# Optimization experiments

Hardware: AMD Instinct MI355X
Metric: run time of the kernel (lower is better)

Reference implementation:

```python
import jax, jax.numpy as jnp
import numpy as np

B, S, E, H = 2, 2048, 768, 8
D = E // H  # 96
SCALING = D ** (-0.5)


def setup_inputs() -> dict:
    key = jax.random.key(0)
    ks = jax.random.split(key, 7)
    sd = E ** -0.5
    return {
        "x": jax.random.normal(ks[0], (B, S, E), jnp.float32),
        "Wq": jax.random.normal(ks[1], (E, E), jnp.float32) * sd,
        "bq": jax.random.normal(ks[2], (E,), jnp.float32) * 0.02,
        "Wk": jax.random.normal(ks[3], (E, E), jnp.float32) * sd,
        "bk": jax.random.normal(ks[4], (E,), jnp.float32) * 0.02,
        "Wo": jax.random.normal(ks[5], (E, E), jnp.float32) * sd,
        "bo": jax.random.normal(ks[6], (E,), jnp.float32) * 0.02,
    }


def _split_heads(t):
    # [B, S, E] -> [B, H, S, D]
    return t.reshape(B, S, H, D).transpose(0, 2, 1, 3)


def reference(x, Wq, bq, Wk, bk, Wo, bo):
    q = _split_heads(x @ Wq + bq)
    k = _split_heads(x @ Wk + bk)
    # NOTE: faithful to source bug — values use the KEY projection
    v = _split_heads(x @ Wk + bk)
    energies = jnp.einsum("bhqd,bhkd->bhqk", q, k)  # [B,H,S,S]
    # NOTE: faithful to source — scaling applied AFTER softmax
    attn = jax.nn.softmax(energies, axis=-1) * SCALING
    out = jnp.einsum("bhqk,bhkd->bhqd", attn, v)
    out = out.transpose(0, 2, 1, 3).reshape(B, S, E)
    return out @ Wo + bo
```

## Files before the change

kernel.cpp:

```cpp
#include <hip/hip_runtime.h>
#include <hip/hip_bf16.h>
#include <math.h>
#include <stdint.h>

#define B_DIM 2
#define S_DIM 2048
#define E_DIM 768
#define H_DIM 8
#define D_DIM 96
#define M_DIM (B_DIM*S_DIM)
#define SCALE_F 0.10206207261596575f
#define LOG2E_F 1.44269504088896341f

typedef _Float16 f16x8 __attribute__((ext_vector_type(8)));
typedef float    f32x4  __attribute__((ext_vector_type(4)));
typedef float    f32x16 __attribute__((ext_vector_type(16)));
typedef unsigned int u32x4 __attribute__((ext_vector_type(4)));

#define MFMA16H(a,b,c) __builtin_amdgcn_mfma_f32_16x16x32_f16(a,b,c,0,0,0)
#define MFMA32H(a,b,c) __builtin_amdgcn_mfma_f32_32x32x16_f16(a,b,c,0,0,0)

__device__ inline unsigned short f2h(float f) {
    return __builtin_bit_cast(unsigned short, (_Float16)f);
}

__device__ inline unsigned pk2(float a, float b) {
    return __builtin_bit_cast(unsigned, __builtin_amdgcn_cvt_pkrtz(a, b));
}

__device__ inline void gload16(const void* g, void* l) {
    auto gp = reinterpret_cast<const __attribute__((address_space(1))) uint32_t*>(
        reinterpret_cast<uintptr_t>(g));
    auto lp = reinterpret_cast<__attribute__((address_space(3))) uint32_t*>(
        reinterpret_cast<uintptr_t>(l));
    __builtin_amdgcn_global_load_lds(gp, lp, 16, 0, 0);
}

__global__ __launch_bounds__(256) void prep_kernel(
    const float* __restrict__ X,
    const float* __restrict__ W0, const float* __restrict__ W1,
    const float* __restrict__ W2,
    unsigned short* __restrict__ Xf,
    unsigned short* __restrict__ T0, unsigned short* __restrict__ T1,
    unsigned short* __restrict__ T2)
{
    const int tid = threadIdx.x;
    if (blockIdx.x < 3072) {
        int i = (blockIdx.x * 256 + tid) * 4;
        float4 v = *(const float4*)(X + i);
        ushort4 h;
        h.x = f2h(v.x); h.y = f2h(v.y); h.z = f2h(v.z); h.w = f2h(v.w);
        *(ushort4*)(Xf + i) = h;
        return;
    }
    int idx = blockIdx.x - 3072;
    int z = idx / 144, rem = idx % 144;
    const float* W; unsigned short* T;
    if (z == 0)      { W = W0; T = T0; }
    else if (z == 1) { W = W1; T = T1; }
    else             { W = W2; T = T2; }
    const float sc = (z == 0) ? LOG2E_F : 1.0f;
    int k0 = (rem / 12) << 6, n0 = (rem % 12) << 6;

    __shared__ float tile[64][65];
    const int r = tid >> 4, c4 = (tid & 15) << 2;
    #pragma unroll
    for (int i = 0; i < 4; ++i) {
        float4 v = *(const float4*)(W + (size_t)(k0 + r + i*16)*E_DIM + n0 + c4);
        tile[r + i*16][c4+0] = v.x; tile[r + i*16][c4+1] = v.y;
        tile[r + i*16][c4+2] = v.z; tile[r + i*16][c4+3] = v.w;
    }
    __syncthreads();
    #pragma unroll
    for (int i = 0; i < 4; ++i) {
        int n = r + i*16;
        ushort4 h;
        h.x = f2h(tile[c4+0][n] * sc); h.y = f2h(tile[c4+1][n] * sc);
        h.z = f2h(tile[c4+2][n] * sc); h.w = f2h(tile[c4+3][n] * sc);
        *(ushort4*)(T + (size_t)(n0 + n)*E_DIM + k0 + c4) = h;
    }
}

__global__ __launch_bounds__(256) void gemm_qk_kernel(
    const unsigned short* __restrict__ A, const unsigned short* __restrict__ Bt,
    const float* __restrict__ bq, const float* __restrict__ bk,
    unsigned short* __restrict__ Qf, unsigned short* __restrict__ Kf)
{
    __shared__ unsigned short sA[2*8192];
    __shared__ unsigned short sB[2*4096];

    const int tid  = threadIdx.x;
    const int lane = tid & 63;
    const int w    = tid >> 6;
    const int qn   = lane & 15, quad = lane >> 4;
    const int wm   = w & 1, wn = w >> 1;

    const int flat = blockIdx.x;
    const int g = flat & 7, s = flat >> 3;
    const int row0 = ((g << 2) + (s & 3)) << 7;
    const int col0 = (s >> 2) << 6;

    const int ar = tid >> 2;
    const int ak = (tid & 3) << 3;

    const unsigned short* gA = A  + (size_t)(row0 + ar)*E_DIM + ak;
    const unsigned short* gB = Bt + (size_t)(col0 + ar)*E_DIM + ak;

    f32x4 acc[4][2];
    #pragma unroll
    for (int mt = 0; mt < 4; ++mt)
        #pragma unroll
        for (int nt = 0; nt < 2; ++nt)
            { acc[mt][nt][0]=0.f; acc[mt][nt][1]=0.f; acc[mt][nt][2]=0.f; acc[mt][nt][3]=0.f; }

    gload16(gA,                 sA + tid*8);
    gload16(gA + 64*E_DIM,      sA + 2048 + tid*8);
    gload16(gA + 32,            sA + 4096 + tid*8);
    gload16(gA + 64*E_DIM + 32, sA + 6144 + tid*8);
    gload16(gB,                 sB + tid*8);
    gload16(gB + 32,            sB + 2048 + tid*8);
    __syncthreads();

    for (int it = 0; it < 12; ++it) {
        const int cur = it & 1, nb = cur ^ 1;
        if (it < 11) {
            const int kn = (it + 1) << 6;
            gload16(gA + kn,                 sA + nb*8192 + tid*8);
            gload16(gA + 64*E_DIM + kn,      sA + nb*8192 + 2048 + tid*8);
            gload16(gA + kn + 32,            sA + nb*8192 + 4096 + tid*8);
            gload16(gA + 64*E_DIM + kn + 32, sA + nb*8192 + 6144 + tid*8);
            gload16(gB + kn,                 sB + nb*4096 + tid*8);
            gload16(gB + kn + 32,            sB + nb*4096 + 2048 + tid*8);
        }

        #pragma unroll
        for (int kk = 0; kk < 2; ++kk) {
            f16x8 af[4], bf[2];
            #pragma unroll
            for (int mt = 0; mt < 4; ++mt)
                af[mt] = *(const f16x8*)
                    &sA[cur*8192 + kk*4096 + (wm*64 + mt*16 + qn)*32 + quad*8];
            #pragma unroll
            for (int nt = 0; nt < 2; ++nt)
                bf[nt] = *(const f16x8*)
                    &sB[cur*4096 + kk*2048 + (wn*32 + nt*16 + qn)*32 + quad*8];
            #pragma unroll
            for (int mt = 0; mt < 4; ++mt)
                #pragma unroll
                for (int nt = 0; nt < 2; ++nt)
                    acc[mt][nt] = MFMA16H(af[mt], bf[nt], acc[mt][nt]);
        }
        __syncthreads();
    }

    #pragma unroll
    for (int nt = 0; nt < 2; ++nt) {
        int n = col0 + wn*32 + nt*16 + qn;
        bool isQ = n < E_DIM;
        float bias = isQ ? bq[n] * LOG2E_F : bk[n - E_DIM];
        unsigned short* op = isQ ? Qf : Kf;
        int nc = isQ ? n : n - E_DIM;
        #pragma unroll
        for (int mt = 0; mt < 4; ++mt)
            #pragma unroll
            for (int r = 0; r < 4; ++r) {
                int m = row0 + wm*64 + mt*16 + quad*4 + r;
                op[(size_t)m*E_DIM + nc] = f2h(acc[mt][nt][r] + bias);
            }
    }
}

__global__ __launch_bounds__(256) void attn_mfma_kernel(
    const unsigned short* __restrict__ Qf, const unsigned short* __restrict__ Kf,
    unsigned short* __restrict__ O0, unsigned short* __restrict__ O1,
    float2* __restrict__ ml)
{
    __shared__ unsigned short sKh[2][64][104];
    __shared__ unsigned short sKt[2][96][72];

    const int tid  = threadIdx.x;
    const int w    = tid >> 6;
    const int lane = tid & 63;
    const int col  = lane & 31;
    const int half = lane >> 5;
    const int b    = blockIdx.z >> 1;
    const int kh   = blockIdx.z & 1;
    const int h    = blockIdx.y;
    const int q0   = blockIdx.x << 7;
    const int key0 = kh << 10;

    f16x8 qf[6];
    {
        const size_t ro = ((size_t)(b*S_DIM + q0 + w*32 + col))*E_DIM
                          + h*D_DIM + half*8;
        #pragma unroll
        for (int kc = 0; kc < 6; ++kc)
            qf[kc] = *(const f16x8*)(Qf + ro + kc*16);
    }

    f32x16 o[3];
    #pragma unroll
    for (int nt = 0; nt < 3; ++nt)
        #pragma unroll
        for (int r = 0; r < 16; ++r) o[nt][r] = 0.f;
    float m_i = -INFINITY, l_i = 0.f;

    const bool stager = tid < 128;
    const int st = tid & 127;
    const int sp = st >> 2;
    const int dq = st & 3;
    const int kp2 = ((sp + ((dq & 1) << 4)) & 31) << 1;

    uint4 r0[3], r1[3];
    if (stager) {
        const size_t g0 = ((size_t)(b*S_DIM + key0 + 2*sp))*E_DIM + h*D_DIM + dq*8;
        #pragma unroll
        for (int i = 0; i < 3; ++i) {
            r0[i] = *(const uint4*)(Kf + g0 + 32*i);
            r1[i] = *(const uint4*)(Kf + g0 + E_DIM + 32*i);
        }
    }

    const int kswz = ((col >> 3) & 1) << 2;

    for (int kt = 0; kt < 16; ++kt) {
        const int p = kt & 1;
        if (stager) {
            #pragma unroll
            for (int i = 0; i < 3; ++i) {
                *(uint4*)&sKh[p][2*sp  ][dq*8 + 32*i] = r0[i];
                *(uint4*)&sKh[p][2*sp+1][dq*8 + 32*i] = r1[i];
            }
            const unsigned short* p0 = (const unsigned short*)r0;
            const unsigned short* p1 = (const unsigned short*)r1;
            #pragma unroll
            for (int c = 0; c < 24; ++c) {
                int d = dq*8 + ((c >> 3) << 5) + (c & 7);
                unsigned pk = (unsigned)p0[c] | ((unsigned)p1[c] << 16);
                *(unsigned*)&sKt[p][d][kp2] = pk;
            }
        }
        __syncthreads();

        if (stager && kt + 1 < 16) {
            const size_t g0 = ((size_t)(b*S_DIM + key0 + (kt+1)*64 + 2*sp))*E_DIM
                              + h*D_DIM + dq*8;
            #pragma unroll
            for (int i = 0; i < 3; ++i) {
                r0[i] = *(const uint4*)(Kf + g0 + 32*i);
                r1[i] = *(const uint4*)(Kf + g0 + E_DIM + 32*i);
            }
        }

        f32x16 s[2];
        __builtin_amdgcn_s_setprio(1);
        #pragma unroll
        for (int mt = 0; mt < 2; ++mt) {
            f32x16 acc;
            #pragma unroll
            for (int r = 0; r < 16; ++r) acc[r] = 0.f;
            #pragma unroll
            for (int kc = 0; kc < 6; ++kc) {
                f16x8 ah = *(const f16x8*)&sKh[p][mt*32 + col][kc*16 + half*8];
                acc = MFMA32H(ah, qf[kc], acc);
            }
            s[mt] = acc;
        }
        __builtin_amdgcn_s_setprio(0);

        float t[8];
        #pragma unroll
        for (int r = 0; r < 8; ++r)
            t[r] = fmaxf(fmaxf(s[0][r], s[0][r+8]), fmaxf(s[1][r], s[1][r+8]));
        float mx = fmaxf(fmaxf(fmaxf(t[0], t[1]), fmaxf(t[2], t[3])),
                         fmaxf(fmaxf(t[4], t[5]), fmaxf(t[6], t[7])));
        mx = fmaxf(mx, __shfl_xor(mx, 32));

        if (__any(mx > m_i + 10.0f)) {
            float m_new = fmaxf(m_i, mx);
            float alpha = __builtin_amdgcn_exp2f(m_i - m_new);
            l_i *= alpha;
            #pragma unroll
            for (int nt = 0; nt < 3; ++nt)
                #pragma unroll
                for (int r = 0; r < 16; ++r) o[nt][r] *= alpha;
            m_i = m_new;
        }

        #pragma unroll
        for (int mt = 0; mt < 2; ++mt)
            #pragma unroll
            for (int r = 0; r < 16; ++r)
                s[mt][r] = __builtin_amdgcn_exp2f(s[mt][r] - m_i);

        float a[8];
        #pragma unroll
        for (int r = 0; r < 8; ++r)
            a[r] = (s[0][r] + s[0][r+8]) + (s[1][r] + s[1][r+8]);
        float ps = ((a[0]+a[1]) + (a[2]+a[3])) + ((a[4]+a[5]) + (a[6]+a[7]));
        ps += __shfl_xor(ps, 32);
        l_i = l_i + ps;

        __builtin_amdgcn_s_setprio(1);
        #pragma unroll
        for (int kc = 0; kc < 4; ++kc) {
            const int mt = kc >> 1;
            const int g0 = (kc & 1) << 3;
            unsigned A0 = pk2(s[mt][g0+0], s[mt][g0+1]);
            unsigned A1 = pk2(s[mt][g0+2], s[mt][g0+3]);
            unsigned B0 = pk2(s[mt][g0+4], s[mt][g0+5]);
            unsigned B1 = pk2(s[mt][g0+6], s[mt][g0+7]);
            auto w0 = __builtin_amdgcn_permlane32_swap(A0, B0, false, false);
            auto w1 = __builtin_amdgcn_permlane32_swap(A1, B1, false, false);
            u32x4 pw;
            pw[0] = w0[0]; pw[1] = w1[0]; pw[2] = w0[1]; pw[3] = w1[1];
            f16x8 pb = __builtin_bit_cast(f16x8, pw);
            #pragma unroll
            for (int nt = 0; nt < 3; ++nt) {
                f16x8 va = *(const f16x8*)
                    &sKt[p][nt*32 + col][(((kc << 1) | half) ^ kswz) << 3];
                o[nt] = MFMA32H(va, pb, o[nt]);
            }
        }
        __builtin_amdgcn_s_setprio(0);
    }

    float inv = 1.0f / l_i;
    unsigned short* Ob = (kh ? O1 : O0)
        + ((size_t)(b*S_DIM + q0 + w*32 + col))*E_DIM + h*D_DIM;
    #pragma unroll
    for (int nt = 0; nt < 3; ++nt)
        #pragma unroll
        for (int rg = 0; rg < 4; ++rg) {
            ushort4 pk;
            pk.x = f2h(o[nt][4*rg+0]*inv); pk.y = f2h(o[nt][4*rg+1]*inv);
            pk.z = f2h(o[nt][4*rg+2]*inv); pk.w = f2h(o[nt][4*rg+3]*inv);
            *(ushort4*)(Ob + nt*32 + 8*rg + 4*half) = pk;
        }
    if (lane < 32) {
        int q = q0 + w*32 + lane;
        ml[((size_t)(kh*B_DIM + b)*H_DIM + h)*S_DIM + q] = make_float2(m_i, l_i);
    }
}

__device__ inline float2 mkscale(const float2* __restrict__ ml, int m, int h) {
    int b = m >> 11, q = m & (S_DIM - 1);
    float2 e0 = ml[((size_t)b*H_DIM + h)*S_DIM + q];
    float2 e1 = ml[((size_t)(B_DIM + b)*H_DIM + h)*S_DIM + q];
    float mm = fmaxf(e0.x, e1.x);
    float w0 = e0.y * __builtin_amdgcn_exp2f(e0.x - mm);
    float w1 = e1.y * __builtin_amdgcn_exp2f(e1.x - mm);
    float inv = SCALE_F / (w0 + w1);
    return make_float2(w0*inv, w1*inv);
}

__global__ __launch_bounds__(256) void gemm_out_kernel(
    const unsigned short* __restrict__ O0, const unsigned short* __restrict__ O1,
    const float2* __restrict__ ml, const unsigned short* __restrict__ Bt,
    const float* __restrict__ bo, float* __restrict__ out)
{
    __shared__ unsigned short sA[2*4096];
    __shared__ unsigned short sB[2*4096];

    const int tid  = threadIdx.x;
    const int lane = tid & 63;
    const int w    = tid >> 6;
    const int qn   = lane & 15, quad = lane >> 4;
    const int wm   = w & 1, wn = w >> 1;

    const int flat = blockIdx.x;
    const int g = flat & 7, s = flat >> 3;
    const int row0 = ((g << 3) + (s & 7)) << 6;
    const int col0 = (s >> 3) << 6;

    const int ar = tid >> 2;
    const int ak = (tid & 3) << 3;

    const size_t r0o = (size_t)(row0 + ar)*E_DIM;
    const unsigned short* gB = Bt + (size_t)(col0 + ar)*E_DIM + ak;

    f32x4 acc[2][2];
    #pragma unroll
    for (int mt = 0; mt < 2; ++mt)
        #pragma unroll
        for (int nt = 0; nt < 2; ++nt)
            { acc[mt][nt][0]=0.f; acc[mt][nt][1]=0.f; acc[mt][nt][2]=0.f; acc[mt][nt][3]=0.f; }

    f16x8 uA = *(const f16x8*)(O0 + r0o + ak);
    f16x8 vA = *(const f16x8*)(O1 + r0o + ak);
    f16x8 uB = *(const f16x8*)(O0 + r0o + 32 + ak);
    f16x8 vB = *(const f16x8*)(O1 + r0o + 32 + ak);
    int hA = 0, hB = 0;
    float2 s2 = mkscale(ml, row0 + ar, 0);
    _Float16 axA = (_Float16)s2.x, ayA = (_Float16)s2.y;
    _Float16 axB = axA, ayB = ayA;

    {
        f16x8 c0 = uA * axA + vA * ayA;
        f16x8 c1 = uB * axB + vB * ayB;
        *(f16x8*)&sA[       ar*32 + ak] = c0;
        *(f16x8*)&sA[2048 + ar*32 + ak] = c1;
        gload16(gB,      sB + tid*8);
        gload16(gB + 32, sB + 2048 + tid*8);
    }
    __syncthreads();

    for (int it = 0; it < 12; ++it) {
        const int cur = it & 1, nb = cur ^ 1;
        const bool hasNext = it < 11;
        const int kn = (it + 1) << 6;

        if (hasNext) {
            gload16(gB + kn,      sB + nb*4096 + tid*8);
            gload16(gB + kn + 32, sB + nb*4096 + 2048 + tid*8);
            uA = *(const f16x8*)(O0 + r0o + kn + ak);
            vA = *(const f16x8*)(O1 + r0o + kn + ak);
            uB = *(const f16x8*)(O0 + r0o + kn + 32 + ak);
            vB = *(const f16x8*)(O1 + r0o + kn + 32 + ak);
        }

        #pragma unroll
        for (int kk = 0; kk < 2; ++kk) {
            f16x8 af[2], bf[2];
            #pragma unroll
            for (int mt = 0; mt < 2; ++mt)
                af[mt] = *(const f16x8*)
                    &sA[cur*4096 + kk*2048 + (wm*32 + mt*16 + qn)*32 + quad*8];
            #pragma unroll
            for (int nt = 0; nt < 2; ++nt)
                bf[nt] = *(const f16x8*)
                    &sB[cur*4096 + kk*2048 + (wn*32 + nt*16 + qn)*32 + quad*8];
            #pragma unroll
            for (int mt = 0; mt < 2; ++mt)
                #pragma unroll
                for (int nt = 0; nt < 2; ++nt)
                    acc[mt][nt] = MFMA16H(af[mt], bf[nt], acc[mt][nt]);
        }

        if (hasNext) {
            int nhA = kn / D_DIM, nhB = (kn + 32) / D_DIM;
            if (nhA != hA) {
                float2 t = mkscale(ml, row0 + ar, nhA);
                axA = (_Float16)t.x; ayA = (_Float16)t.y; hA = nhA;
            }
            if (nhB != hB) {
                float2 t = mkscale(ml, row0 + ar, nhB);
                axB = (_Float16)t.x; ayB = (_Float16)t.y; hB = nhB;
            }
            f16x8 c0 = uA * axA + vA * ayA;
            f16x8 c1 = uB * axB + vB * ayB;
            *(f16x8*)&sA[nb*4096 +        ar*32 + ak] = c0;
            *(f16x8*)&sA[nb*4096 + 2048 + ar*32 + ak] = c1;
        }
        __syncthreads();
    }

    #pragma unroll
    for (int nt = 0; nt < 2; ++nt) {
        int n = col0 + wn*32 + nt*16 + qn;
        float bias = bo[n];
        #pragma unroll
        for (int mt = 0; mt < 2; ++mt)
            #pragma unroll
            for (int r = 0; r < 4; ++r) {
                int m = row0 + wm*32 + mt*16 + quad*4 + r;
                out[(size_t)m*E_DIM + n] = acc[mt][nt][r] + bias;
            }
    }
}

extern "C" void kernel_launch(void* const* d_in, const int* in_sizes, int n_in,
                              void* d_out, int out_size, void* d_ws, size_t ws_size,
                              hipStream_t stream)
{
    const float* x  = (const float*)d_in[0];
    const float* Wq = (const float*)d_in[1];
    const float* bq = (const float*)d_in[2];
    const float* Wk = (const float*)d_in[3];
    const float* bk = (const float*)d_in[4];
    const float* Wo = (const float*)d_in[5];
    const float* bo = (const float*)d_in[6];
    float* out = (float*)d_out;

    const size_t NE = (size_t)M_DIM * E_DIM;
    const size_t WE = (size_t)E_DIM * E_DIM;
    unsigned short* xf    = (unsigned short*)d_ws;
    unsigned short* WqkT  = xf + NE;
    unsigned short* WoT   = WqkT + 2*WE;
    unsigned short* Qf    = WoT + WE;
    unsigned short* Kf    = Qf + NE;
    unsigned short* Oh1   = Kf + NE;
    float2*         mlbuf = (float2*)(Oh1 + NE);
    unsigned short* Oh0   = xf;

    dim3 blk(256);
    hipLaunchKernelGGL(prep_kernel, dim3(3504), blk, 0, stream,
                       x, Wq, Wk, Wo, xf, WqkT, WqkT + WE, WoT);

    hipLaunchKernelGGL(gemm_qk_kernel, dim3(768), blk, 0, stream,
                       xf, WqkT, bq, bk, Qf, Kf);

    hipLaunchKernelGGL(attn_mfma_kernel, dim3(S_DIM/128, H_DIM, B_DIM*2), blk, 0,
                       stream, Qf, Kf, Oh0, Oh1, mlbuf);

    hipLaunchKernelGGL(gemm_out_kernel, dim3(768), blk, 0, stream,
                       Oh0, Oh1, mlbuf, WoT, bo, out);
}
```

Before: 150.9 us.

## Software-pipeline attention loop: compute next tile's QK^T while softmax/PV of current

```diff
diff --git a/kernel.cpp b/kernel.cpp
--- a/kernel.cpp
+++ b/kernel.cpp
@@ -223,9 +223,55 @@
 
     const int kswz = ((col >> 3) & 1) << 2;
 
-    for (int kt = 0; kt < 16; ++kt) {
+    f32x16 sc[2];
+
+    if (stager) {
+        #pragma unroll
+        for (int i = 0; i < 3; ++i) {
+            *(uint4*)&sKh[0][2*sp  ][dq*8 + 32*i] = r0[i];
+            *(uint4*)&sKh[0][2*sp+1][dq*8 + 32*i] = r1[i];
+        }
+        const unsigned short* p0 = (const unsigned short*)r0;
+        const unsigned short* p1 = (const unsigned short*)r1;
+        #pragma unroll
+        for (int c = 0; c < 24; ++c) {
+            int d = dq*8 + ((c >> 3) << 5) + (c & 7);
+            unsigned pk = (unsigned)p0[c] | ((unsigned)p1[c] << 16);
+            *(unsigned*)&sKt[0][d][kp2] = pk;
+        }
+    }
+    __syncthreads();
+    if (stager) {
+        const size_t g0 = ((size_t)(b*S_DIM + key0 + 64 + 2*sp))*E_DIM
+                          + h*D_DIM + dq*8;
+        #pragma unroll
+        for (int i = 0; i < 3; ++i) {
+            r0[i] = *(const uint4*)(Kf + g0 + 32*i);
+            r1[i] = *(const uint4*)(Kf + g0 + E_DIM + 32*i);
+        }
+    }
+    __builtin_amdgcn_s_setprio(1);
+    #pragma unroll
+    for (int mt = 0; mt < 2; ++mt) {
+        f32x16 acc;
+        #pragma unroll
+        for (int r = 0; r < 16; ++r) acc[r] = 0.f;
+        #pragma unroll
+        for (int kc = 0; kc < 6; ++kc) {
+            f16x8 ah = *(const f16x8*)&sKh[0][mt*32 + col][kc*16 + half*8];
+            acc = MFMA32H(ah, qf[kc], acc);
+        }
+        sc[mt] = acc;
+    }
+    __builtin_amdgcn_s_setprio(0);
+    __syncthreads();
+
+    #pragma unroll 2
+    for (int kt = 1; kt <= 16; ++kt) {
         const int p = kt & 1;
-        if (stager) {
+        const bool has = (kt < 16);
+
+        if (has && stager) {
             #pragma unroll
             for (int i = 0; i < 3; ++i) {
                 *(uint4*)&sKh[p][2*sp  ][dq*8 + 32*i] = r0[i];
@@ -242,7 +288,7 @@
         }
         __syncthreads();
 
-        if (stager && kt + 1 < 16) {
+        if (stager && kt < 15) {
             const size_t g0 = ((size_t)(b*S_DIM + key0 + (kt+1)*64 + 2*sp))*E_DIM
                               + h*D_DIM + dq*8;
             #pragma unroll
@@ -252,26 +298,28 @@
             }
         }
 
-        f32x16 s[2];
         __builtin_amdgcn_s_setprio(1);
-        #pragma unroll
-        for (int mt = 0; mt < 2; ++mt) {
-            f32x16 acc;
-            #pragma unroll
-            for (int r = 0; r < 16; ++r) acc[r] = 0.f;
-            #pragma unroll
-            for (int kc = 0; kc < 6; ++kc) {
-                f16x8 ah = *(const f16x8*)&sKh[p][mt*32 + col][kc*16 + half*8];
-                acc = MFMA32H(ah, qf[kc], acc);
-            }
-            s[mt] = acc;
-        }
-        __builtin_amdgcn_s_setprio(0);
+
+        f32x16 sn[2];
+        if (has) {
+            #pragma unroll
+            for (int mt = 0; mt < 2; ++mt) {
+                f32x16 acc;
+                #pragma unroll
+                for (int r = 0; r < 16; ++r) acc[r] = 0.f;
+                #pragma unroll
+                for (int kc = 0; kc < 6; ++kc) {
+                    f16x8 ah = *(const f16x8*)&sKh[p][mt*32 + col][kc*16 + half*8];
+                    acc = MFMA32H(ah, qf[kc], acc);
+                }
+                sn[mt] = acc;
+            }
+        }
 
         float t[8];
         #pragma unroll
         for (int r = 0; r < 8; ++r)
-            t[r] = fmaxf(fmaxf(s[0][r], s[0][r+8]), fmaxf(s[1][r], s[1][r+8]));
+            t[r] = fmaxf(fmaxf(sc[0][r], sc[0][r+8]), fmaxf(sc[1][r], sc[1][r+8]));
         float mx = fmaxf(fmaxf(fmaxf(t[0], t[1]), fmaxf(t[2], t[3])),
                          fmaxf(fmaxf(t[4], t[5]), fmaxf(t[6], t[7])));
         mx = fmaxf(mx, __shfl_xor(mx, 32));
@@ -291,25 +339,24 @@
         for (int mt = 0; mt < 2; ++mt)
             #pragma unroll
             for (int r = 0; r < 16; ++r)
-                s[mt][r] = __builtin_amdgcn_exp2f(s[mt][r] - m_i);
+                sc[mt][r] = __builtin_amdgcn_exp2f(sc[mt][r] - m_i);
 
         float a[8];
         #pragma unroll
         for (int r = 0; r < 8; ++r)
-            a[r] = (s[0][r] + s[0][r+8]) + (s[1][r] + s[1][r+8]);
+            a[r] = (sc[0][r] + sc[0][r+8]) + (sc[1][r] + sc[1][r+8]);
         float ps = ((a[0]+a[1]) + (a[2]+a[3])) + ((a[4]+a[5]) + (a[6]+a[7]));
         ps += __shfl_xor(ps, 32);
         l_i = l_i + ps;
 
-        __builtin_amdgcn_s_setprio(1);
         #pragma unroll
         for (int kc = 0; kc < 4; ++kc) {
             const int mt = kc >> 1;
             const int g0 = (kc & 1) << 3;
-            unsigned A0 = pk2(s[mt][g0+0], s[mt][g0+1]);
-            unsigned A1 = pk2(s[mt][g0+2], s[mt][g0+3]);
-            unsigned B0 = pk2(s[mt][g0+4], s[mt][g0+5]);
-            unsigned B1 = pk2(s[mt][g0+6], s[mt][g0+7]);
+            unsigned A0 = pk2(sc[mt][g0+0], sc[mt][g0+1]);
+            unsigned A1 = pk2(sc[mt][g0+2], sc[mt][g0+3]);
+            unsigned B0 = pk2(sc[mt][g0+4], sc[mt][g0+5]);
+            unsigned B1 = pk2(sc[mt][g0+6], sc[mt][g0+7]);
             auto w0 = __builtin_amdgcn_permlane32_swap(A0, B0, false, false);
             auto w1 = __builtin_amdgcn_permlane32_swap(A1, B1, false, false);
             u32x4 pw;
@@ -318,11 +365,15 @@
             #pragma unroll
             for (int nt = 0; nt < 3; ++nt) {
                 f16x8 va = *(const f16x8*)
-                    &sKt[p][nt*32 + col][(((kc << 1) | half) ^ kswz) << 3];
+                    &sKt[p^1][nt*32 + col][(((kc << 1) | half) ^ kswz) << 3];
                 o[nt] = MFMA32H(va, pb, o[nt]);
             }
         }
         __builtin_amdgcn_s_setprio(0);
+
+        if (has) { sc[0] = sn[0]; sc[1] = sn[1]; }
+
+        __syncthreads();
     }
 
     float inv = 1.0f / l_i;
```

Result: slower. 169.7 us (+12.4%).
